# Performance work log

Measured on AMD Instinct MI355X. Metric: run time of the kernel, lower is better.

The kernel has to match this reference:

```python
import jax, jax.numpy as jnp
import numpy as np

M, K, N = 2048, 4096, 8192
BITS = 4
GROUP_SIZE = 128
G = K // GROUP_SIZE  # 32 groups
PACK = 8 // BITS     # 2 values per int8 byte


def setup_inputs() -> dict:
    key = jax.random.key(0)
    k_a, k_q, k_s = jax.random.split(key, 3)
    A = jax.random.normal(k_a, (M, K), dtype=jnp.float16)
    # packed 4-bit weights: each byte stores two uint4 values (low nibble first)
    qweight = jax.random.randint(k_q, (N, K // PACK), 0, 256, dtype=jnp.int32)
    scales = jax.random.normal(k_s, (N, G), dtype=jnp.float16)
    zeros = jnp.zeros((N, G), dtype=jnp.float16)
    bias = jnp.zeros((N,), dtype=jnp.float16)
    return {"A": A, "qweight": qweight, "scales": scales, "zeros": zeros, "bias": bias}


def _dequantize(qweight, scales, zeros):
    # unpack two uint4 values per byte (low nibble is the earlier element)
    q = qweight.astype(jnp.int32)
    lo = q & 0xF
    hi = (q >> 4) & 0xF
    intw = jnp.stack([lo, hi], axis=-1).reshape(N, K)  # [N, K] uint4 values
    # zeros_mode='original': w = (q - zero) * scale, per group of GROUP_SIZE
    wq = intw.reshape(N, G, GROUP_SIZE).astype(jnp.float16)
    w = (wq - zeros[:, :, None]) * scales[:, :, None]
    return w.reshape(N, K)


def reference(A, qweight, scales, zeros, bias):
    W = _dequantize(qweight, scales, zeros)          # [N, K] fp16
    out = jnp.einsum('mk,nk->mn', A, W) + bias       # 'nt' layout: A @ W^T + bias
    return out.astype(A.dtype)
```

## Files before the change

### kernel.cpp

```cpp
#include <hip/hip_runtime.h>
#include <stdint.h>

#define MDIM 2048
#define KDIM 4096
#define NDIM 8192
#define NG   32
#define QROW 2048
#define NT2  64
#define LSTR 36
#define BUFH 32768

typedef __attribute__((ext_vector_type(4))) float    f32x4;
typedef __attribute__((ext_vector_type(2))) _Float16 f16x2;
typedef __attribute__((ext_vector_type(8))) _Float16 f16x8;
typedef __attribute__((ext_vector_type(4))) int      i32x4;

#define CVT2(a,b) __builtin_bit_cast(f16x2, __builtin_amdgcn_cvt_pkrtz((a),(b)))
#define BCU(x)    __builtin_bit_cast(unsigned, (x))
#define BCH2(x)   __builtin_bit_cast(f16x2, (x))
#define MFMA16(A,B,C) __builtin_amdgcn_mfma_f32_16x16x32_f16((A),(B),(C),0,0,0)
#define LDSREAD(DST, OFF) __builtin_memcpy(&(DST), &lds[(OFF)], 16)

__device__ __forceinline__ void gload_lds16(const void* g, void* l) {
  __builtin_amdgcn_global_load_lds(
      (const __attribute__((address_space(1))) void*)g,
      (__attribute__((address_space(3))) void*)l, 16, 0, 0);
}

__device__ __forceinline__ uint4 dequant8(i32x4 q, float sf, float zf) {
  const _Float16 sh = (_Float16)sf;
  const _Float16 bh = (_Float16)(-zf * sf);
  const f16x2 s2 = {sh, sh}, b2 = {bh, bh};
  const f16x2 k2 = {(_Float16)1024.0f, (_Float16)1024.0f};
  uint4 r;
#define DQE(QV, DST) do {                                                   \
    unsigned Bb_ = (unsigned)(QV) & 0xFFu;                                  \
    unsigned bits_ = ((Bb_ | (Bb_ << 12)) & 0x000F000Fu) | 0x64006400u;     \
    DST = BCU((f16x2)((BCH2(bits_) - k2) * s2 + b2));                       \
  } while (0)
  DQE(q.x, r.x); DQE(q.y, r.y); DQE(q.z, r.z); DQE(q.w, r.w);
#undef DQE
  return r;
}

__global__ __launch_bounds__(256) void dequant_w_kernel(
    const int* __restrict__ qw, const float* __restrict__ scales,
    const float* __restrict__ zeros, _Float16* __restrict__ Wf)
{
  const size_t total = (size_t)NDIM * (KDIM / 8);
  for (size_t t = (size_t)blockIdx.x * blockDim.x + threadIdx.x; t < total;
       t += (size_t)gridDim.x * blockDim.x) {
    i32x4 q;
    __builtin_memcpy(&q, qw + 4 * t, 16);
    const int n = (int)(t >> 9);
    const int k = (int)((t & 511) << 3);
    const int g = k >> 7;
    uint4 w = dequant8(q, scales[n * NG + g], zeros[n * NG + g]);
    __builtin_memcpy(Wf + (size_t)n * KDIM + k, &w, 16);
  }
}

__global__ __launch_bounds__(256) void conv_a_kernel(
    const float* __restrict__ A, _Float16* __restrict__ Af)
{
  const size_t total = (size_t)MDIM * (KDIM / 8);
  for (size_t t = (size_t)blockIdx.x * blockDim.x + threadIdx.x; t < total;
       t += (size_t)gridDim.x * blockDim.x) {
    f32x4 v0, v1;
    __builtin_memcpy(&v0, A + 8 * t,     16);
    __builtin_memcpy(&v1, A + 8 * t + 4, 16);
    uint4 h;
    h.x = BCU(CVT2(v0.x, v0.y));
    h.y = BCU(CVT2(v0.z, v0.w));
    h.z = BCU(CVT2(v1.x, v1.y));
    h.w = BCU(CVT2(v1.z, v1.w));
    __builtin_memcpy(Af + 8 * t, &h, 16);
  }
}

__global__ __launch_bounds__(512) void gemm_f16_kernel(
    const _Float16* __restrict__ Af,
    const _Float16* __restrict__ Wf,
    const float* __restrict__ bias,
    float* __restrict__ out)
{
  __shared__ __align__(16) _Float16 lds[2 * BUFH];

  const int tid  = threadIdx.x;
  const int wave = tid >> 6;
  const int lane = tid & 63;
  const int n0 = blockIdx.x << 8;
  const int m0 = blockIdx.y << 8;
  const int wm = (wave >> 2) << 7;
  const int wn = (wave & 3) << 6;

  f32x4 acc[8][4] = {};

  const int srow   = tid >> 3;
  const int schunk = (tid & 7) ^ ((tid >> 3) & 7);
  const _Float16* aU0 = Af + (size_t)(m0 + srow) * KDIM + schunk * 8;
  const _Float16* aU1 = aU0 + (size_t)64 * KDIM;
  const _Float16* aU2 = aU0 + (size_t)128 * KDIM;
  const _Float16* aU3 = aU0 + (size_t)192 * KDIM;
  const _Float16* bU0 = Wf + (size_t)(n0 + srow) * KDIM + schunk * 8;
  const _Float16* bU1 = bU0 + (size_t)64 * KDIM;
  const _Float16* bU2 = bU0 + (size_t)128 * KDIM;
  const _Float16* bU3 = bU0 + (size_t)192 * KDIM;

#define STAGE_P1(X) do {                                               \
    _Float16* d_ = &lds[((X) & 1) * BUFH + (wave << 9)];               \
    const size_t ko_ = (size_t)(X) << 6;                               \
    gload_lds16(aU0 + ko_, d_);                                        \
    gload_lds16(aU1 + ko_, d_ + 4096);                                 \
  } while (0)
#define STAGE_P2(X) do {                                               \
    _Float16* d_ = &lds[((X) & 1) * BUFH + (wave << 9)];               \
    const size_t ko_ = (size_t)(X) << 6;                               \
    gload_lds16(aU2 + ko_, d_ + 8192);                                 \
    gload_lds16(aU3 + ko_, d_ + 12288);                                \
  } while (0)
#define STAGE_P3(X) do {                                               \
    _Float16* d_ = &lds[((X) & 1) * BUFH + (wave << 9)];               \
    const size_t ko_ = (size_t)(X) << 6;                               \
    gload_lds16(bU0 + ko_, d_ + 16384);                                \
    gload_lds16(bU1 + ko_, d_ + 20480);                                \
  } while (0)
#define STAGE_P4(X) do {                                               \
    _Float16* d_ = &lds[((X) & 1) * BUFH + (wave << 9)];               \
    const size_t ko_ = (size_t)(X) << 6;                               \
    gload_lds16(bU2 + ko_, d_ + 24576);                                \
    gload_lds16(bU3 + ko_, d_ + 28672);                                \
  } while (0)

  const int fr = lane & 15;
  const int h4 = lane >> 4;
  const int ck0 = (((0 + h4) ^ (fr & 7))) << 3;
  const int ck1 = (((4 + h4) ^ (fr & 7))) << 3;
  int raOff[8], rbOff[4];
#pragma unroll
  for (int i = 0; i < 8; ++i) raOff[i] = (wm + 16 * i + fr) * 64;
#pragma unroll
  for (int j = 0; j < 4; ++j) rbOff[j] = 16384 + (wn + 16 * j + fr) * 64;

#define COMPUTE(T) do {                                                \
    const int bb_ = ((T) & 1) * BUFH;                                  \
    f16x8 b0_[4], b1_[4];                                              \
    _Pragma("unroll")                                                  \
    for (int j = 0; j < 4; ++j) {                                      \
      LDSREAD(b0_[j], bb_ + rbOff[j] + ck0);                           \
      LDSREAD(b1_[j], bb_ + rbOff[j] + ck1);                           \
    }                                                                  \
    _Pragma("unroll")                                                  \
    for (int i = 0; i < 8; ++i) {                                      \
      f16x8 a0_, a1_;                                                  \
      LDSREAD(a0_, bb_ + raOff[i] + ck0);                              \
      LDSREAD(a1_, bb_ + raOff[i] + ck1);                              \
      _Pragma("unroll")                                                \
      for (int j = 0; j < 4; ++j)                                      \
        acc[i][j] = MFMA16(a0_, b0_[j], acc[i][j]);                    \
      _Pragma("unroll")                                                \
      for (int j = 0; j < 4; ++j)                                      \
        acc[i][j] = MFMA16(a1_, b1_[j], acc[i][j]);                    \
    }                                                                  \
  } while (0)

#define PH_MFMA(R) do {                                                \
    __builtin_amdgcn_s_setprio(1);                                     \
    _Pragma("unroll")                                                  \
    for (int j = 0; j < 4; ++j) {                                      \
      acc[(R)][j]     = MFMA16(aA0, bf0[j], acc[(R)][j]);              \
      acc[(R) + 1][j] = MFMA16(aB0, bf0[j], acc[(R) + 1][j]);          \
    }                                                                  \
    _Pragma("unroll")                                                  \
    for (int j = 0; j < 4; ++j) {                                      \
      acc[(R)][j]     = MFMA16(aA1, bf1[j], acc[(R)][j]);              \
      acc[(R) + 1][j] = MFMA16(aB1, bf1[j], acc[(R) + 1][j]);          \
    }                                                                  \
    __builtin_amdgcn_s_setprio(0);                                     \
  } while (0)

#define RD_A(I)                                                        \
    LDSREAD(aA0, bb + raOff[I] + ck0);                                 \
    LDSREAD(aA1, bb + raOff[I] + ck1);                                 \
    LDSREAD(aB0, bb + raOff[(I) + 1] + ck0);                           \
    LDSREAD(aB1, bb + raOff[(I) + 1] + ck1);

  STAGE_P1(0); STAGE_P2(0); STAGE_P3(0); STAGE_P4(0);
  STAGE_P1(1);

#pragma clang loop unroll(disable)
  for (int t = 0; t < NT2 - 2; ++t) {
    asm volatile("s_waitcnt vmcnt(2)" ::: "memory");
    __builtin_amdgcn_s_barrier();
    const int bb = (t & 1) * BUFH;

    f16x8 bf0[4], bf1[4], aA0, aA1, aB0, aB1;

#pragma unroll
    for (int j = 0; j < 4; ++j) {
      LDSREAD(bf0[j], bb + rbOff[j] + ck0);
      LDSREAD(bf1[j], bb + rbOff[j] + ck1);
    }
    RD_A(0)
    STAGE_P2(t + 1);
    PH_MFMA(0);

    RD_A(2)
    STAGE_P3(t + 1);
    PH_MFMA(2);

    RD_A(4)
    STAGE_P4(t + 1);
    PH_MFMA(4);

    RD_A(6)
    __builtin_amdgcn_s_barrier();
    STAGE_P1(t + 2);
    PH_MFMA(6);
  }

  STAGE_P2(NT2 - 1); STAGE_P3(NT2 - 1); STAGE_P4(NT2 - 1);
  asm volatile("s_waitcnt vmcnt(8)" ::: "memory");
  __builtin_amdgcn_s_barrier();
  COMPUTE(NT2 - 2);
  asm volatile("s_waitcnt vmcnt(0)" ::: "memory");
  __builtin_amdgcn_s_barrier();
  COMPUTE(NT2 - 1);

#undef STAGE_P1
#undef STAGE_P2
#undef STAGE_P3
#undef STAGE_P4
#undef COMPUTE
#undef PH_MFMA
#undef RD_A

  const int cr = (lane >> 4) << 2;
  const int cc = lane & 15;
#pragma unroll
  for (int j = 0; j < 4; ++j) {
    const int n = n0 + wn + j * 16 + cc;
    const float bv = bias[n];
#pragma unroll
    for (int i = 0; i < 8; ++i) {
      const int mrow = m0 + wm + i * 16 + cr;
#pragma unroll
      for (int r = 0; r < 4; ++r)
        out[(size_t)(mrow + r) * NDIM + n] = acc[i][j][r] + bv;
    }
  }
}

__global__ __launch_bounds__(256, 4) void qlin_fused_kernel(
    const float* __restrict__ A, const int* __restrict__ qw,
    const float* __restrict__ scales, const float* __restrict__ zeros,
    const float* __restrict__ bias, float* __restrict__ out)
{
  __shared__ _Float16 As[2][128 * LSTR];
  __shared__ _Float16 Bs[2][128 * LSTR];

  const int tid  = threadIdx.x;
  const int wave = tid >> 6;
  const int lane = tid & 63;
  const int n0 = blockIdx.x << 7;
  const int m0 = blockIdx.y << 7;
  const int wm = (wave >> 1) << 6;
  const int wn = (wave & 1) << 6;

  f32x4 acc[4][4] = {};

  const int r4 = tid >> 2;
  const int c4 = tid & 3;

  const float* aP0 = A + (size_t)(m0 + r4) * KDIM + c4 * 8;
  const float* aP1 = aP0 + (size_t)64 * KDIM;
  const int*   qP0 = qw + (size_t)(n0 + r4) * QROW + c4 * 4;
  const int*   qP1 = qP0 + (size_t)64 * QROW;
  const float* sP0 = scales + (size_t)(n0 + r4) * NG;
  const float* zP0 = zeros  + (size_t)(n0 + r4) * NG;
  const float* sP1 = sP0 + (size_t)64 * NG;
  const float* zP1 = zP0 + (size_t)64 * NG;

  const int aD0 = r4 * LSTR + c4 * 8;
  const int aD1 = (r4 + 64) * LSTR + c4 * 8;

  const int fr = lane & 15;
  const int k0 = (lane >> 4) * 8;
  const int ra0 = (wm +  0 + fr) * LSTR + k0;
  const int ra1 = (wm + 16 + fr) * LSTR + k0;
  const int ra2 = (wm + 32 + fr) * LSTR + k0;
  const int ra3 = (wm + 48 + fr) * LSTR + k0;
  const int rb0 = (wn +  0 + fr) * LSTR + k0;
  const int rb1 = (wn + 16 + fr) * LSTR + k0;
  const int rb2 = (wn + 32 + fr) * LSTR + k0;
  const int rb3 = (wn + 48 + fr) * LSTR + k0;

  f32x4 pa0, pa1, pa2, pa3;
  i32x4 pq0, pq1;
  float psf0, pzf0, psf1, pzf1;

#define ISSUE(KT) do {                                                        \
    __builtin_memcpy(&pa0, aP0 + (size_t)(KT) * 32,     16);                  \
    __builtin_memcpy(&pa1, aP0 + (size_t)(KT) * 32 + 4, 16);                  \
    __builtin_memcpy(&pa2, aP1 + (size_t)(KT) * 32,     16);                  \
    __builtin_memcpy(&pa3, aP1 + (size_t)(KT) * 32 + 4, 16);                  \
    __builtin_memcpy(&pq0, qP0 + (size_t)(KT) * 16, 16);                      \
    __builtin_memcpy(&pq1, qP1 + (size_t)(KT) * 16, 16);                      \
    const int g_ = (KT) >> 2;                                                 \
    psf0 = sP0[g_]; pzf0 = zP0[g_];                                           \
    psf1 = sP1[g_]; pzf1 = zP1[g_];                                           \
  } while (0)

#define STAGE(P) do {                                                         \
    uint4 aw0_;                                                               \
    aw0_.x = BCU(CVT2(pa0.x, pa0.y));                                         \
    aw0_.y = BCU(CVT2(pa0.z, pa0.w));                                         \
    aw0_.z = BCU(CVT2(pa1.x, pa1.y));                                         \
    aw0_.w = BCU(CVT2(pa1.z, pa1.w));                                         \
    __builtin_memcpy(&As[P][aD0], &aw0_, 16);                                 \
    uint4 aw1_;                                                               \
    aw1_.x = BCU(CVT2(pa2.x, pa2.y));                                         \
    aw1_.y = BCU(CVT2(pa2.z, pa2.w));                                         \
    aw1_.z = BCU(CVT2(pa3.x, pa3.y));                                         \
    aw1_.w = BCU(CVT2(pa3.z, pa3.w));                                         \
    __builtin_memcpy(&As[P][aD1], &aw1_, 16);                                 \
    uint4 bw0_ = dequant8(pq0, psf0, pzf0);                                   \
    __builtin_memcpy(&Bs[P][aD0], &bw0_, 16);                                 \
    uint4 bw1_ = dequant8(pq1, psf1, pzf1);                                   \
    __builtin_memcpy(&Bs[P][aD1], &bw1_, 16);                                 \
  } while (0)

#define COMPUTE(P) do {                                                       \
    f16x8 af[4], bfr[4];                                                      \
    __builtin_memcpy(&af[0], &As[P][ra0], 16);                                \
    __builtin_memcpy(&af[1], &As[P][ra1], 16);                                \
    __builtin_memcpy(&af[2], &As[P][ra2], 16);                                \
    __builtin_memcpy(&af[3], &As[P][ra3], 16);                                \
    __builtin_memcpy(&bfr[0], &Bs[P][rb0], 16);                               \
    __builtin_memcpy(&bfr[1], &Bs[P][rb1], 16);                               \
    __builtin_memcpy(&bfr[2], &Bs[P][rb2], 16);                               \
    __builtin_memcpy(&bfr[3], &Bs[P][rb3], 16);                               \
    _Pragma("unroll")                                                         \
    for (int i = 0; i < 4; ++i)                                               \
      _Pragma("unroll")                                                       \
      for (int j = 0; j < 4; ++j)                                             \
        acc[i][j] = MFMA16(af[i], bfr[j], acc[i][j]);                         \
  } while (0)

  ISSUE(0);
  STAGE(0);
  __syncthreads();

#pragma clang loop unroll(disable)
  for (int kt = 0; kt < 127; ++kt) {
    const int p = kt & 1;
    ISSUE(kt + 1);
    COMPUTE(p);
    STAGE(p ^ 1);
    __syncthreads();
  }
  COMPUTE(1);

#undef ISSUE
#undef STAGE
#undef COMPUTE

  const int cr = (lane >> 4) << 2;
  const int cc = lane & 15;
#pragma unroll
  for (int j = 0; j < 4; ++j) {
    const int n = n0 + wn + j * 16 + cc;
    const float bv = bias[n];
#pragma unroll
    for (int i = 0; i < 4; ++i) {
      const int mrow = m0 + wm + i * 16 + cr;
#pragma unroll
      for (int r = 0; r < 4; ++r)
        out[(size_t)(mrow + r) * NDIM + n] = acc[i][j][r] + bv;
    }
  }
}

extern "C" void kernel_launch(void* const* d_in, const int* in_sizes, int n_in,
                              void* d_out, int out_size, void* d_ws, size_t ws_size,
                              hipStream_t stream) {
  const float* A      = (const float*)d_in[0];
  const int*   qwp    = (const int*)d_in[1];
  const float* scales = (const float*)d_in[2];
  const float* zerosp = (const float*)d_in[3];
  const float* biasp  = (const float*)d_in[4];
  float*       outp   = (float*)d_out;

  const size_t needW = (size_t)NDIM * KDIM * sizeof(_Float16);
  const size_t needA = (size_t)MDIM * KDIM * sizeof(_Float16);

  if (ws_size >= needW + needA) {
    _Float16* Wf = (_Float16*)d_ws;
    _Float16* Af = (_Float16*)((char*)d_ws + needW);
    dequant_w_kernel<<<2048, 256, 0, stream>>>(qwp, scales, zerosp, Wf);
    conv_a_kernel<<<2048, 256, 0, stream>>>(A, Af);
    dim3 grid(NDIM / 256, MDIM / 256);
    gemm_f16_kernel<<<grid, 512, 0, stream>>>(Af, Wf, biasp, outp);
  } else {
    dim3 grid(NDIM / 128, MDIM / 128);
    qlin_fused_kernel<<<grid, 256, 0, stream>>>(A, qwp, scales, zerosp, biasp, outp);
  }
}
```

Measured before the change: 155.1 us.

## Fuse weight dequantization into GEMM mainloop, removing separate dequant kernel

Removes the standalone dequant kernel that wrote a full fp16 weight matrix to workspace. The GEMM now loads packed int4 weights into registers, dequantizes them in the loop, and writes the fp16 values into swizzled LDS itself. A still uses async global-to-LDS loads. The pipeline is reshaped around this: B is issued one tile ahead, waited on with vmcnt, and written after the last A read, with one fewer barrier per iteration. This saves a kernel launch and a large write-then-read of the fp16 weights, but adds ALU and LDS-store work, and register pressure, inside the GEMM loop.

```diff
diff --git a/kernel.cpp b/kernel.cpp
--- a/kernel.cpp
+++ b/kernel.cpp
@@ -41,23 +41,6 @@
   DQE(q.x, r.x); DQE(q.y, r.y); DQE(q.z, r.z); DQE(q.w, r.w);
 #undef DQE
   return r;
-}
-
-__global__ __launch_bounds__(256) void dequant_w_kernel(
-    const int* __restrict__ qw, const float* __restrict__ scales,
-    const float* __restrict__ zeros, _Float16* __restrict__ Wf)
-{
-  const size_t total = (size_t)NDIM * (KDIM / 8);
-  for (size_t t = (size_t)blockIdx.x * blockDim.x + threadIdx.x; t < total;
-       t += (size_t)gridDim.x * blockDim.x) {
-    i32x4 q;
-    __builtin_memcpy(&q, qw + 4 * t, 16);
-    const int n = (int)(t >> 9);
-    const int k = (int)((t & 511) << 3);
-    const int g = k >> 7;
-    uint4 w = dequant8(q, scales[n * NG + g], zeros[n * NG + g]);
-    __builtin_memcpy(Wf + (size_t)n * KDIM + k, &w, 16);
-  }
 }
 
 __global__ __launch_bounds__(256) void conv_a_kernel(
@@ -78,11 +61,13 @@
   }
 }
 
-__global__ __launch_bounds__(512) void gemm_f16_kernel(
+__global__ __launch_bounds__(512) void gemm_q_kernel(
     const _Float16* __restrict__ Af,
-    const _Float16* __restrict__ Wf,
-    const float* __restrict__ bias,
-    float* __restrict__ out)
+    const int*      __restrict__ qw,
+    const float*    __restrict__ scales,
+    const float*    __restrict__ zeros,
+    const float*    __restrict__ bias,
+    float*          __restrict__ out)
 {
   __shared__ __align__(16) _Float16 lds[2 * BUFH];
 
@@ -102,34 +87,52 @@
   const _Float16* aU1 = aU0 + (size_t)64 * KDIM;
   const _Float16* aU2 = aU0 + (size_t)128 * KDIM;
   const _Float16* aU3 = aU0 + (size_t)192 * KDIM;
-  const _Float16* bU0 = Wf + (size_t)(n0 + srow) * KDIM + schunk * 8;
-  const _Float16* bU1 = bU0 + (size_t)64 * KDIM;
-  const _Float16* bU2 = bU0 + (size_t)128 * KDIM;
-  const _Float16* bU3 = bU0 + (size_t)192 * KDIM;
-
-#define STAGE_P1(X) do {                                               \
+
+#define STAGE_A2a(X) do {                                              \
     _Float16* d_ = &lds[((X) & 1) * BUFH + (wave << 9)];               \
     const size_t ko_ = (size_t)(X) << 6;                               \
     gload_lds16(aU0 + ko_, d_);                                        \
     gload_lds16(aU1 + ko_, d_ + 4096);                                 \
   } while (0)
-#define STAGE_P2(X) do {                                               \
+#define STAGE_A2b(X) do {                                              \
     _Float16* d_ = &lds[((X) & 1) * BUFH + (wave << 9)];               \
     const size_t ko_ = (size_t)(X) << 6;                               \
     gload_lds16(aU2 + ko_, d_ + 8192);                                 \
     gload_lds16(aU3 + ko_, d_ + 12288);                                \
   } while (0)
-#define STAGE_P3(X) do {                                               \
-    _Float16* d_ = &lds[((X) & 1) * BUFH + (wave << 9)];               \
-    const size_t ko_ = (size_t)(X) << 6;                               \
-    gload_lds16(bU0 + ko_, d_ + 16384);                                \
-    gload_lds16(bU1 + ko_, d_ + 20480);                                \
-  } while (0)
-#define STAGE_P4(X) do {                                               \
-    _Float16* d_ = &lds[((X) & 1) * BUFH + (wave << 9)];               \
-    const size_t ko_ = (size_t)(X) << 6;                               \
-    gload_lds16(bU2 + ko_, d_ + 24576);                                \
-    gload_lds16(bU3 + ko_, d_ + 28672);                                \
+
+  const int brow = tid >> 1;
+  const int bkc  = tid & 1;
+  const int bsw  = brow & 7;
+  const int*   qB = qw + (size_t)(n0 + brow) * QROW + bkc * 16;
+  const float* sB = scales + (size_t)(n0 + brow) * NG;
+  const float* zB = zeros  + (size_t)(n0 + brow) * NG;
+
+  i32x4 bq0, bq1, bq2, bq3;
+  float bs, bz;
+
+#define ISSUE_B(X) do {                                                \
+    const int* q_ = qB + (size_t)(X) * 32;                             \
+    __builtin_memcpy(&bq0, q_,      16);                               \
+    __builtin_memcpy(&bq1, q_ + 4,  16);                               \
+    __builtin_memcpy(&bq2, q_ + 8,  16);                               \
+    __builtin_memcpy(&bq3, q_ + 12, 16);                               \
+    const int g_ = (X) >> 1;                                           \
+    __builtin_memcpy(&bs, sB + g_, 4);                                 \
+    __builtin_memcpy(&bz, zB + g_, 4);                                 \
+  } while (0)
+
+#define WRITE_B(X) do {                                                \
+    _Float16* db_ = &lds[((X) & 1) * BUFH + 16384 + brow * 64];        \
+    uint4 w_;                                                          \
+    w_ = dequant8(bq0, bs, bz);                                        \
+    __builtin_memcpy(db_ + ((4 * bkc + 0) ^ bsw) * 8, &w_, 16);        \
+    w_ = dequant8(bq1, bs, bz);                                        \
+    __builtin_memcpy(db_ + ((4 * bkc + 1) ^ bsw) * 8, &w_, 16);        \
+    w_ = dequant8(bq2, bs, bz);                                        \
+    __builtin_memcpy(db_ + ((4 * bkc + 2) ^ bsw) * 8, &w_, 16);        \
+    w_ = dequant8(bq3, bs, bz);                                        \
+    __builtin_memcpy(db_ + ((4 * bkc + 3) ^ bsw) * 8, &w_, 16);        \
   } while (0)
 
   const int fr = lane & 15;
@@ -185,12 +188,16 @@
     LDSREAD(aB0, bb + raOff[(I) + 1] + ck0);                           \
     LDSREAD(aB1, bb + raOff[(I) + 1] + ck1);
 
-  STAGE_P1(0); STAGE_P2(0); STAGE_P3(0); STAGE_P4(0);
-  STAGE_P1(1);
+  ISSUE_B(0);
+  STAGE_A2a(0); STAGE_A2b(0);
+  asm volatile("s_waitcnt vmcnt(4)" ::: "memory");
+  WRITE_B(0);
+  asm volatile("s_waitcnt lgkmcnt(0)" ::: "memory");
 
 #pragma clang loop unroll(disable)
-  for (int t = 0; t < NT2 - 2; ++t) {
-    asm volatile("s_waitcnt vmcnt(2)" ::: "memory");
+  for (int t = 0; t < NT2 - 1; ++t) {
+    ISSUE_B(t + 1);
+    asm volatile("s_waitcnt vmcnt(6)" ::: "memory");
     __builtin_amdgcn_s_barrier();
     const int bb = (t & 1) * BUFH;
 
@@ -202,35 +209,31 @@
       LDSREAD(bf1[j], bb + rbOff[j] + ck1);
     }
     RD_A(0)
-    STAGE_P2(t + 1);
+    STAGE_A2a(t + 1);
     PH_MFMA(0);
 
     RD_A(2)
-    STAGE_P3(t + 1);
+    STAGE_A2b(t + 1);
     PH_MFMA(2);
 
     RD_A(4)
-    STAGE_P4(t + 1);
     PH_MFMA(4);
 
     RD_A(6)
-    __builtin_amdgcn_s_barrier();
-    STAGE_P1(t + 2);
+    asm volatile("s_waitcnt vmcnt(4)" ::: "memory");
+    WRITE_B(t + 1);
     PH_MFMA(6);
-  }
-
-  STAGE_P2(NT2 - 1); STAGE_P3(NT2 - 1); STAGE_P4(NT2 - 1);
-  asm volatile("s_waitcnt vmcnt(8)" ::: "memory");
-  __builtin_amdgcn_s_barrier();
-  COMPUTE(NT2 - 2);
+    asm volatile("s_waitcnt lgkmcnt(0)" ::: "memory");
+  }
+
   asm volatile("s_waitcnt vmcnt(0)" ::: "memory");
   __builtin_amdgcn_s_barrier();
   COMPUTE(NT2 - 1);
 
-#undef STAGE_P1
-#undef STAGE_P2
-#undef STAGE_P3
-#undef STAGE_P4
+#undef STAGE_A2a
+#undef STAGE_A2b
+#undef ISSUE_B
+#undef WRITE_B
 #undef COMPUTE
 #undef PH_MFMA
 #undef RD_A
@@ -391,16 +394,13 @@
   const float* biasp  = (const float*)d_in[4];
   float*       outp   = (float*)d_out;
 
-  const size_t needW = (size_t)NDIM * KDIM * sizeof(_Float16);
   const size_t needA = (size_t)MDIM * KDIM * sizeof(_Float16);
 
-  if (ws_size >= needW + needA) {
-    _Float16* Wf = (_Float16*)d_ws;
-    _Float16* Af = (_Float16*)((char*)d_ws + needW);
-    dequant_w_kernel<<<2048, 256, 0, stream>>>(qwp, scales, zerosp, Wf);
+  if (ws_size >= needA) {
+    _Float16* Af = (_Float16*)d_ws;
     conv_a_kernel<<<2048, 256, 0, stream>>>(A, Af);
     dim3 grid(NDIM / 256, MDIM / 256);
-    gemm_f16_kernel<<<grid, 512, 0, stream>>>(Af, Wf, biasp, outp);
+    gemm_q_kernel<<<grid, 512, 0, stream>>>(Af, qwp, scales, zerosp, biasp, outp);
   } else {
     dim3 grid(NDIM / 128, MDIM / 128);
     qlin_fused_kernel<<<grid, 256, 0, stream>>>(A, qwp, scales, zerosp, biasp, outp);
```

Measured after the change: 162.2 us. +4.6%, slower.
